# Optimization experiments

Hardware: AMD Instinct MI355X
Metric: run time of the kernel (lower is better)

The kernel has to match this reference:

```python
import jax, jax.numpy as jnp
import numpy as np

SHIFT = 1  # module picks random +-1 at init; fixed deterministically to +1


def setup_inputs() -> dict:
    key = jax.random.key(0)
    k1, k2, k3 = jax.random.split(key, 3)
    x = jax.random.normal(k1, (128, 128, 56, 56), dtype=jnp.float32)
    w0 = jax.random.normal(k2, (2, 3, 3, 32), dtype=jnp.float32)
    w1 = jax.random.normal(k3, (64, 4), dtype=jnp.float32)
    return {"x": x, "w0": w0, "w1": w1}


def _unfold3(t, axis):
    # F.unfold with kernel (3,1), padding (1,0) along `axis` (length 56):
    # zero-pad by 1 on each side, then stack the 3 shifted windows as a new
    # axis placed just BEFORE `axis` (matching torch's C*kh channel ordering
    # after the reshapes in the original module).
    pad = [(0, 0)] * t.ndim
    pad[axis] = (1, 1)
    p = jnp.pad(t, pad)
    slices = []
    for a in range(3):
        idx = [slice(None)] * t.ndim
        idx[axis] = slice(a, a + 56)
        slices.append(p[tuple(idx)])
    return jnp.stack(slices, axis=axis)


def reference(x, w0, w1):
    # x: (128,128,56,56) -> (k=128, j=64, m=2, n=56, l=56)
    t3 = x.reshape(128, 64, 2, 56, 56)
    # channel mix: contract j=64 against w1 (64,4) -> (b, m=2, n=56, l=56, i=4)
    t4 = jnp.einsum('kjmnl,ji->kmnli', t3, w1)
    # first unfold over l (axis 3): (b, 2, 56, kA=3, l=56, i=4)
    u1 = _unfold3(t4, axis=3)
    # second unfold over l again (now axis 4), padding applied to u1 (which
    # already contains zeros from the first padding) -> (b,2,56,kA,kB,l,i)
    u2 = _unfold3(u1, axis=4)
    # torch permute (0,1,2,5,4,3,6): (b, 2, 56, l, kB, kA, i)
    t5 = jnp.transpose(u2, (0, 1, 2, 5, 4, 3, 6))
    # conv-like contraction with w0 (l=2, i=3, k=3, j=32) -> (b,56,56,4,32)
    t6 = jnp.einsum('mlonikp,likj->monpj', t5, w0)
    # (b,56,56,32,4) -> (b,56,56,128), roll along H, -> NCHW
    t7 = jnp.transpose(t6, (0, 1, 2, 4, 3)).reshape(128, 56, 56, 128)
    t7 = jnp.roll(t7, SHIFT, axis=1)
    return jnp.transpose(t7, (0, 3, 1, 2))
```

## Files before the change

kernel.cpp:

```cpp
#include <hip/hip_runtime.h>

namespace {
constexpr int HH = 56, WW = 56;
constexpr int CPLANE = HH * WW;

__global__ __launch_bounds__(256, 2) void fused_kernel(
    const float* __restrict__ x,
    const float* __restrict__ w0,
    const float* __restrict__ w1,
    float* __restrict__ out)
{
    __shared__ float  ls[14][9][60];
    __shared__ float  Wc[32][2][5];
    __shared__ float  fx0[32][2], fx3[32][2];
    __shared__ float4 w1s[64];

    const int tid = threadIdx.x;
    const int b   = blockIdx.x >> 2;
    const int h0  = (blockIdx.x & 3) * 14;

    if (tid < 64) w1s[tid] = ((const float4*)w1)[tid];

    if (tid >= 64 && tid < 128) {
        const int j = (tid - 64) >> 1, m = (tid - 64) & 1;
        float w[3][3];
        #pragma unroll
        for (int kB = 0; kB < 3; ++kB)
            #pragma unroll
            for (int kA = 0; kA < 3; ++kA)
                w[kB][kA] = w0[((m * 3 + kB) * 3 + kA) * 32 + j];
        Wc[j][m][0] = w[0][0];
        Wc[j][m][1] = w[0][1] + w[1][0];
        Wc[j][m][2] = w[0][2] + w[1][1] + w[2][0];
        Wc[j][m][3] = w[1][2] + w[2][1];
        Wc[j][m][4] = w[2][2];
        fx0[j][m] = w[0][2];
        fx3[j][m] = w[2][0];
    }

    if (tid < 224) {
        const int row  = tid >> 1;
        const int half = tid & 1;
        *(float2*)&ls[row >> 3][row & 7][half ? 58 : 0] = make_float2(0.f, 0.f);
    }

    __syncthreads();

    const int  rh = tid / 14;
    const int  wq = tid - rh * 14;
    const int  l0 = 4 * wq;
    const bool active = (tid < 196);

    if (active) {
        const float* xp = x + ((size_t)b * 128 * HH + (h0 + rh)) * WW + l0;
        float acc[2][4][4] = {};
        float4 pA[8], pB[8];

        auto LOADG = [&](float4* buf, int c0) {
            #pragma unroll
            for (int k = 0; k < 8; ++k)
                buf[k] = *(const float4*)(xp + (size_t)(c0 + k) * CPLANE);
        };
        auto FMA8 = [&](const float4* buf, int c0) {
            #pragma unroll
            for (int k = 0; k < 8; ++k) {
                const int m = k & 1;
                const float4 wv = w1s[(c0 + k) >> 1];
                const float xk[4] = {buf[k].x, buf[k].y, buf[k].z, buf[k].w};
                const float wk[4] = {wv.x, wv.y, wv.z, wv.w};
                #pragma unroll
                for (int i = 0; i < 4; ++i)
                    #pragma unroll
                    for (int q = 0; q < 4; ++q)
                        acc[m][i][q] = fmaf(xk[q], wk[i], acc[m][i][q]);
            }
        };

        LOADG(pA, 0);
        #pragma unroll
        for (int c0 = 0; c0 < 112; c0 += 16) {
            LOADG(pB, c0 + 8);
            FMA8(pA, c0);
            LOADG(pA, c0 + 16);
            FMA8(pB, c0 + 8);
        }
        LOADG(pB, 120);
        FMA8(pA, 112);
        FMA8(pB, 120);

        #pragma unroll
        for (int m = 0; m < 2; ++m)
            #pragma unroll
            for (int i = 0; i < 4; ++i) {
                *(float2*)&ls[rh][m * 4 + i][2 + l0]     = make_float2(acc[m][i][0], acc[m][i][1]);
                *(float2*)&ls[rh][m * 4 + i][2 + l0 + 2] = make_float2(acc[m][i][2], acc[m][i][3]);
            }
    }
    __syncthreads();

    if (!active) return;

    float v[2][4][8];
    #pragma unroll
    for (int m = 0; m < 2; ++m)
        #pragma unroll
        for (int i = 0; i < 4; ++i) {
            const float* p = &ls[rh][m * 4 + i][l0];
            const float4 p0 = *(const float4*)p;
            const float4 p1 = *(const float4*)(p + 4);
            v[m][i][0] = p0.x; v[m][i][1] = p0.y; v[m][i][2] = p0.z; v[m][i][3] = p0.w;
            v[m][i][4] = p1.x; v[m][i][5] = p1.y; v[m][i][6] = p1.z; v[m][i][7] = p1.w;
        }

    const int h_out = (h0 + rh + 1) % HH;
    float* obase = out + ((size_t)b * 128 * HH + h_out) * WW + l0;

    #pragma unroll 2
    for (int j = 0; j < 32; ++j) {
        float W[2][5], f0[2], f3[2];
        #pragma unroll
        for (int m = 0; m < 2; ++m) {
            #pragma unroll
            for (int d = 0; d < 5; ++d) W[m][d] = Wc[j][m][d];
            f0[m] = fx0[j][m];
            f3[m] = fx3[j][m];
        }
        #pragma unroll
        for (int i = 0; i < 4; ++i) {
            float o0 = 0.f, o1 = 0.f, o2 = 0.f, o3 = 0.f;
            #pragma unroll
            for (int m = 0; m < 2; ++m)
                #pragma unroll
                for (int d = 0; d < 5; ++d) {
                    const float wd = W[m][d];
                    o0 = fmaf(v[m][i][d],     wd, o0);
                    o1 = fmaf(v[m][i][d + 1], wd, o1);
                    o2 = fmaf(v[m][i][d + 2], wd, o2);
                    o3 = fmaf(v[m][i][d + 3], wd, o3);
                }
            if (wq == 0)  o0 -= v[0][i][2] * f0[0] + v[1][i][2] * f0[1];
            if (wq == 13) o3 -= v[0][i][5] * f3[0] + v[1][i][5] * f3[1];
            *(float4*)(obase + (size_t)(j * 4 + i) * CPLANE) = make_float4(o0, o1, o2, o3);
        }
    }
}
}

extern "C" void kernel_launch(void* const* d_in, const int* in_sizes, int n_in,
                              void* d_out, int out_size, void* d_ws, size_t ws_size,
                              hipStream_t stream) {
    const float* x  = (const float*)d_in[0];
    const float* w0 = (const float*)d_in[1];
    const float* w1 = (const float*)d_in[2];
    float* out = (float*)d_out;
    fused_kernel<<<dim3(128 * 4), dim3(256), 0, stream>>>(x, w0, w1, out);
}
```

Baseline: 131.0 us.

## Split channel reduction across lanes with shuffle reduce, one block per output row

Moves from 512 blocks of 256 threads (14 rows per block) to 7168 blocks of 128 threads, each handling a single H row. The 64-channel w1 contraction is split over 4 lanes per pixel group, each summing 16 channels, and the partial sums are combined with xor-shuffles. The output stage is redistributed so every thread computes 14 (channel, column-group) items. The aim is higher occupancy and more memory parallelism on a bandwidth-bound kernel, at the cost of more blocks, shuffle work and per-block weight setup.

```diff
diff --git a/kernel.cpp b/kernel.cpp
--- a/kernel.cpp
+++ b/kernel.cpp
@@ -4,24 +4,24 @@
 constexpr int HH = 56, WW = 56;
 constexpr int CPLANE = HH * WW;
 
-__global__ __launch_bounds__(256, 2) void fused_kernel(
+__global__ __launch_bounds__(128, 4) void fused_kernel(
     const float* __restrict__ x,
     const float* __restrict__ w0,
     const float* __restrict__ w1,
     float* __restrict__ out)
 {
-    __shared__ float  ls[14][9][60];
+    __shared__ float  t4s[2][4][60];
     __shared__ float  Wc[32][2][5];
     __shared__ float  fx0[32][2], fx3[32][2];
     __shared__ float4 w1s[64];
 
     const int tid = threadIdx.x;
-    const int b   = blockIdx.x >> 2;
-    const int h0  = (blockIdx.x & 3) * 14;
+    const int b   = blockIdx.x / HH;
+    const int h   = blockIdx.x - b * HH;
 
-    if (tid < 64) w1s[tid] = ((const float4*)w1)[tid];
-
-    if (tid >= 64 && tid < 128) {
+    if (tid < 64) {
+        w1s[tid] = ((const float4*)w1)[tid];
+    } else {
         const int j = (tid - 64) >> 1, m = (tid - 64) & 1;
         float w[3][3];
         #pragma unroll
@@ -37,111 +37,106 @@
         fx0[j][m] = w[0][2];
         fx3[j][m] = w[2][0];
     }
-
-    if (tid < 224) {
-        const int row  = tid >> 1;
-        const int half = tid & 1;
-        *(float2*)&ls[row >> 3][row & 7][half ? 58 : 0] = make_float2(0.f, 0.f);
+    if (tid < 16) {
+        const int row = tid >> 1, half = tid & 1;
+        *(float2*)&t4s[row >> 2][row & 3][half ? 58 : 0] = make_float2(0.f, 0.f);
     }
-
     __syncthreads();
 
-    const int  rh = tid / 14;
-    const int  wq = tid - rh * 14;
-    const int  l0 = 4 * wq;
-    const bool active = (tid < 196);
+    if (tid < 112) {
+        const int js = tid & 3;
+        const int m  = (tid >> 2) & 1;
+        const int lq = tid >> 3;
+        const int l0 = lq * 4;
+        const float*  xp = x + ((size_t)(b * 128 + 2 * (js * 16) + m) * HH + h) * WW + l0;
+        const size_t  jstride = (size_t)2 * CPLANE;
 
-    if (active) {
-        const float* xp = x + ((size_t)b * 128 * HH + (h0 + rh)) * WW + l0;
-        float acc[2][4][4] = {};
+        float acc[4][4] = {};
         float4 pA[8], pB[8];
 
-        auto LOADG = [&](float4* buf, int c0) {
+        auto LOADG = [&](float4* buf, int j0) {
             #pragma unroll
             for (int k = 0; k < 8; ++k)
-                buf[k] = *(const float4*)(xp + (size_t)(c0 + k) * CPLANE);
+                buf[k] = *(const float4*)(xp + (size_t)(j0 + k) * jstride);
         };
-        auto FMA8 = [&](const float4* buf, int c0) {
+        auto FMA8 = [&](const float4* buf, int j0) {
             #pragma unroll
             for (int k = 0; k < 8; ++k) {
-                const int m = k & 1;
-                const float4 wv = w1s[(c0 + k) >> 1];
+                const float4 wv = w1s[js * 16 + j0 + k];
                 const float xk[4] = {buf[k].x, buf[k].y, buf[k].z, buf[k].w};
                 const float wk[4] = {wv.x, wv.y, wv.z, wv.w};
                 #pragma unroll
                 for (int i = 0; i < 4; ++i)
                     #pragma unroll
                     for (int q = 0; q < 4; ++q)
-                        acc[m][i][q] = fmaf(xk[q], wk[i], acc[m][i][q]);
+                        acc[i][q] = fmaf(xk[q], wk[i], acc[i][q]);
             }
         };
 
         LOADG(pA, 0);
-        #pragma unroll
-        for (int c0 = 0; c0 < 112; c0 += 16) {
-            LOADG(pB, c0 + 8);
-            FMA8(pA, c0);
-            LOADG(pA, c0 + 16);
-            FMA8(pB, c0 + 8);
-        }
-        LOADG(pB, 120);
-        FMA8(pA, 112);
-        FMA8(pB, 120);
+        LOADG(pB, 8);
+        FMA8(pA, 0);
+        FMA8(pB, 8);
 
         #pragma unroll
-        for (int m = 0; m < 2; ++m)
+        for (int i = 0; i < 4; ++i)
             #pragma unroll
-            for (int i = 0; i < 4; ++i) {
-                *(float2*)&ls[rh][m * 4 + i][2 + l0]     = make_float2(acc[m][i][0], acc[m][i][1]);
-                *(float2*)&ls[rh][m * 4 + i][2 + l0 + 2] = make_float2(acc[m][i][2], acc[m][i][3]);
+            for (int q = 0; q < 4; ++q) {
+                acc[i][q] += __shfl_xor(acc[i][q], 1);
+                acc[i][q] += __shfl_xor(acc[i][q], 2);
             }
+
+        const float o0 = js == 0 ? acc[0][0] : js == 1 ? acc[1][0] : js == 2 ? acc[2][0] : acc[3][0];
+        const float o1 = js == 0 ? acc[0][1] : js == 1 ? acc[1][1] : js == 2 ? acc[2][1] : acc[3][1];
+        const float o2 = js == 0 ? acc[0][2] : js == 1 ? acc[1][2] : js == 2 ? acc[2][2] : acc[3][2];
+        const float o3 = js == 0 ? acc[0][3] : js == 1 ? acc[1][3] : js == 2 ? acc[2][3] : acc[3][3];
+
+        *(float2*)&t4s[m][js][2 + l0]     = make_float2(o0, o1);
+        *(float2*)&t4s[m][js][2 + l0 + 2] = make_float2(o2, o3);
     }
     __syncthreads();
 
-    if (!active) return;
+    const int h_out = (h + 1) % HH;
+    float* ob = out + ((size_t)b * 128 * HH + h_out) * WW;
 
-    float v[2][4][8];
-    #pragma unroll
-    for (int m = 0; m < 2; ++m)
+    #pragma unroll 2
+    for (int it = 0; it < 14; ++it) {
+        const int item = it * 128 + tid;
+        const int c  = item / 14;
+        const int wq = item - c * 14;
+        const int l0 = wq * 4;
+        const int j  = c >> 2;
+        const int i  = c & 3;
+
+        const float* p0 = &t4s[0][i][l0];
+        const float* p1 = &t4s[1][i][l0];
+        const float4 a0 = *(const float4*)p0, b0 = *(const float4*)(p0 + 4);
+        const float4 a1 = *(const float4*)p1, b1 = *(const float4*)(p1 + 4);
+        const float v0[8] = {a0.x, a0.y, a0.z, a0.w, b0.x, b0.y, b0.z, b0.w};
+        const float v1[8] = {a1.x, a1.y, a1.z, a1.w, b1.x, b1.y, b1.z, b1.w};
+
+        float o0 = 0.f, o1 = 0.f, o2 = 0.f, o3 = 0.f;
         #pragma unroll
-        for (int i = 0; i < 4; ++i) {
-            const float* p = &ls[rh][m * 4 + i][l0];
-            const float4 p0 = *(const float4*)p;
-            const float4 p1 = *(const float4*)(p + 4);
-            v[m][i][0] = p0.x; v[m][i][1] = p0.y; v[m][i][2] = p0.z; v[m][i][3] = p0.w;
-            v[m][i][4] = p1.x; v[m][i][5] = p1.y; v[m][i][6] = p1.z; v[m][i][7] = p1.w;
+        for (int d = 0; d < 5; ++d) {
+            const float wd0 = Wc[j][0][d];
+            o0 = fmaf(v0[d],     wd0, o0);
+            o1 = fmaf(v0[d + 1], wd0, o1);
+            o2 = fmaf(v0[d + 2], wd0, o2);
+            o3 = fmaf(v0[d + 3], wd0, o3);
+        }
+        #pragma unroll
+        for (int d = 0; d < 5; ++d) {
+            const float wd1 = Wc[j][1][d];
+            o0 = fmaf(v1[d],     wd1, o0);
+            o1 = fmaf(v1[d + 1], wd1, o1);
+            o2 = fmaf(v1[d + 2], wd1, o2);
+            o3 = fmaf(v1[d + 3], wd1, o3);
         }
 
-    const int h_out = (h0 + rh + 1) % HH;
-    float* obase = out + ((size_t)b * 128 * HH + h_out) * WW + l0;
+        if (wq == 0)  o0 -= v0[2] * fx0[j][0] + v1[2] * fx0[j][1];
+        if (wq == 13) o3 -= v0[5] * fx3[j][0] + v1[5] * fx3[j][1];
 
-    #pragma unroll 2
-    for (int j = 0; j < 32; ++j) {
-        float W[2][5], f0[2], f3[2];
-        #pragma unroll
-        for (int m = 0; m < 2; ++m) {
-            #pragma unroll
-            for (int d = 0; d < 5; ++d) W[m][d] = Wc[j][m][d];
-            f0[m] = fx0[j][m];
-            f3[m] = fx3[j][m];
-        }
-        #pragma unroll
-        for (int i = 0; i < 4; ++i) {
-            float o0 = 0.f, o1 = 0.f, o2 = 0.f, o3 = 0.f;
-            #pragma unroll
-            for (int m = 0; m < 2; ++m)
-                #pragma unroll
-                for (int d = 0; d < 5; ++d) {
-                    const float wd = W[m][d];
-                    o0 = fmaf(v[m][i][d],     wd, o0);
-                    o1 = fmaf(v[m][i][d + 1], wd, o1);
-                    o2 = fmaf(v[m][i][d + 2], wd, o2);
-                    o3 = fmaf(v[m][i][d + 3], wd, o3);
-                }
-            if (wq == 0)  o0 -= v[0][i][2] * f0[0] + v[1][i][2] * f0[1];
-            if (wq == 13) o3 -= v[0][i][5] * f3[0] + v[1][i][5] * f3[1];
-            *(float4*)(obase + (size_t)(j * 4 + i) * CPLANE) = make_float4(o0, o1, o2, o3);
-        }
+        *(float4*)(ob + (size_t)c * CPLANE + l0) = make_float4(o0, o1, o2, o3);
     }
 }
 }
@@ -153,5 +148,5 @@
     const float* w0 = (const float*)d_in[1];
     const float* w1 = (const float*)d_in[2];
     float* out = (float*)d_out;
-    fused_kernel<<<dim3(128 * 4), dim3(256), 0, stream>>>(x, w0, w1, out);
+    fused_kernel<<<dim3(128 * HH), dim3(128), 0, stream>>>(x, w0, w1, out);
 }
```

New measurement: 127.1 us. 1.03x faster.
